# Kernel tuning notes

Hardware: AMD Instinct MI355X
Metric: run time of the kernel (lower is better)

Reference implementation:

```python
import jax, jax.numpy as jnp
import numpy as np
from jax import lax

EPS = 1e-5


def fps(xyz, npoint):
    # Farthest point sampling; xyz [B, N, 3] -> idx [B, npoint] (starts at point 0)
    B, N, _ = xyz.shape

    def body(carry, _):
        dist, far = carry
        c = jnp.take_along_axis(xyz, far[:, None, None], axis=1)  # [B,1,3]
        d = jnp.sum((xyz - c) ** 2, -1)                            # [B,N]
        dist = jnp.minimum(dist, d)
        nxt = jnp.argmax(dist, -1).astype(jnp.int32)
        return (dist, nxt), far

    init = (jnp.full((B, N), 1e10, xyz.dtype), jnp.zeros((B,), jnp.int32))
    _, idx = lax.scan(body, init, None, length=npoint)
    return idx.T  # [B, npoint]


def query_ball(radius, nsample, xyz, new_xyz):
    # xyz [B,N,3], new_xyz [B,S,3] -> idx [B,S,nsample]
    N = xyz.shape[1]
    sqr = jnp.sum((new_xyz[:, :, None, :] - xyz[:, None, :, :]) ** 2, -1)  # [B,S,N]
    idx = jnp.where(sqr > radius * radius, N, jnp.arange(N)[None, None, :])
    idx = jnp.sort(idx, axis=-1)[:, :, :nsample]
    # out-of-ball slots get replaced by the first in-ball index (torch repo behavior)
    return jnp.where(idx == N, idx[:, :, :1], idx)


def gather_pts(x, idx):
    # x [B,N,C], idx [B,...] -> [B,...,C]
    B = x.shape[0]
    b = jnp.arange(B).reshape((B,) + (1,) * (idx.ndim - 1))
    return x[b, idx]


def mlp_bn(x, layers):
    # x [B,S,K,C]; shared 1x1-conv MLP + training-mode BatchNorm + ReLU
    for w, g, b in layers:
        x = jnp.einsum('bskc,oc->bsko', x, w)
        mean = x.mean((0, 1, 2))
        var = x.var((0, 1, 2))  # biased, as torch BN uses for normalization
        x = jax.nn.relu((x - mean) * lax.rsqrt(var + EPS) * g + b)
    return x


def set_abstraction(xyz, points, npoint, radius, nsample, layers, group_all):
    B = xyz.shape[0]
    if group_all:
        new_xyz = jnp.zeros((B, 1, 3), xyz.dtype)
        new_points = xyz[:, None]  # [B,1,N,3] (raw xyz, no centering)
        if points is not None:
            new_points = jnp.concatenate([new_points, points[:, None]], -1)
    else:
        fidx = fps(xyz, npoint)
        new_xyz = gather_pts(xyz, fidx)                     # [B,S,3]
        idx = query_ball(radius, nsample, xyz, new_xyz)     # [B,S,K]
        grouped = gather_pts(xyz, idx) - new_xyz[:, :, None, :]
        if points is not None:
            new_points = jnp.concatenate([grouped, gather_pts(points, idx)], -1)
        else:
            new_points = grouped
    feat = mlp_bn(new_points, layers).max(2)  # max-pool over neighbors -> [B,S,C]
    return new_xyz, feat


def _forward(xyz_time, l1, l2, l3):
    B, T, N, _ = xyz_time.shape
    x = xyz_time.reshape(B * T, N, 4)
    xyz, t = x[..., :3], x[..., 3:]
    x1_xyz, x1 = set_abstraction(xyz, t, 512, 0.2, 32, l1, False)
    x2_xyz, x2 = set_abstraction(x1_xyz, x1, 128, 0.4, 64, l2, False)
    _, x3 = set_abstraction(x2_xyz, x2, None, None, None, l3, True)
    return x3.reshape(B, T, -1)


def setup_inputs() -> dict:
    key = jax.random.key(0)
    ks = jax.random.split(key, 16)
    inp = {"xyz_time": jax.random.uniform(ks[0], (2, 4, 4096, 4), jnp.float32)}
    specs = {1: [(64, 4), (64, 64), (128, 64)],
             2: [(128, 131), (128, 128), (256, 128)],
             3: [(256, 259), (512, 256), (1024, 512)]}
    i = 1
    for s, layers in specs.items():
        for j, (o, c) in enumerate(layers):
            inp[f"w{s}_{j}"] = jax.random.normal(jax.random.fold_in(ks[i], j), (o, c), jnp.float32) * 0.1
            inp[f"g{s}_{j}"] = jnp.ones((o,), jnp.float32)
            inp[f"b{s}_{j}"] = jnp.zeros((o,), jnp.float32)
        i += 1
    return inp


def reference(xyz_time, w1_0, g1_0, b1_0, w1_1, g1_1, b1_1, w1_2, g1_2, b1_2,
              w2_0, g2_0, b2_0, w2_1, g2_1, b2_1, w2_2, g2_2, b2_2,
              w3_0, g3_0, b3_0, w3_1, g3_1, b3_1, w3_2, g3_2, b3_2):
    l1 = [(w1_0, g1_0, b1_0), (w1_1, g1_1, b1_1), (w1_2, g1_2, b1_2)]
    l2 = [(w2_0, g2_0, b2_0), (w2_1, g2_1, b2_1), (w2_2, g2_2, b2_2)]
    l3 = [(w3_0, g3_0, b3_0), (w3_1, g3_1, b3_1), (w3_2, g3_2, b3_2)]
    return _forward(xyz_time, l1, l2, l3)
```

## Files before the change

kernel.cpp:

```cpp
#include <hip/hip_runtime.h>


typedef short s16x8 __attribute__((ext_vector_type(8)));
typedef float f32x4 __attribute__((ext_vector_type(4)));

__device__ __forceinline__ unsigned short f2bf_rne(float f) {
    unsigned u = __float_as_uint(f);
    u += 0x7FFFu + ((u >> 16) & 1u);
    return (unsigned short)(u >> 16);
}
__device__ __forceinline__ void f2bf_split(float v, unsigned short& hi,
                                           unsigned short& lo) {
    unsigned u = __float_as_uint(v);
    unsigned r = u + 0x7FFFu + ((u >> 16) & 1u);
    hi = (unsigned short)(r >> 16);
    float vh = __uint_as_float(r & 0xFFFF0000u);
    lo = f2bf_rne(v - vh);
}

__device__ __forceinline__ unsigned long long umax64(unsigned long long a,
                                                     unsigned long long b) {
    return a > b ? a : b;
}

__device__ __forceinline__ unsigned wred_umax63(unsigned v) {
    unsigned t;
    t = (unsigned)__builtin_amdgcn_update_dpp(0, (int)v, 0x111, 0xf, 0xf, true); if (t > v) v = t;
    t = (unsigned)__builtin_amdgcn_update_dpp(0, (int)v, 0x112, 0xf, 0xf, true); if (t > v) v = t;
    t = (unsigned)__builtin_amdgcn_update_dpp(0, (int)v, 0x114, 0xf, 0xf, true); if (t > v) v = t;
    t = (unsigned)__builtin_amdgcn_update_dpp(0, (int)v, 0x118, 0xf, 0xf, true); if (t > v) v = t;
    t = (unsigned)__builtin_amdgcn_update_dpp(0, (int)v, 0x142, 0xa, 0xf, true); if (t > v) v = t;
    t = (unsigned)__builtin_amdgcn_update_dpp(0, (int)v, 0x143, 0xc, 0xf, true); if (t > v) v = t;
    return v;
}

__device__ __forceinline__ void wave_argmax(unsigned dbits, unsigned nInv,
                                            unsigned& vmax, unsigned& iInv) {
    unsigned m = wred_umax63(dbits);
    vmax = (unsigned)__builtin_amdgcn_readlane((int)m, 63);
    unsigned cand = (dbits == vmax) ? nInv : 0u;
    unsigned im = wred_umax63(cand);
    iInv = (unsigned)__builtin_amdgcn_readlane((int)im, 63);
}

struct PWArgs {
    const float* w[9];
    unsigned off[9];
    int O[9], C[9], CP[9];
};
__device__ __forceinline__ void prep_w_dev(const PWArgs& a,
                                           unsigned short* __restrict__ wh,
                                           unsigned short* __restrict__ wl,
                                           int i) {
    int l = 0;
#pragma unroll
    for (int k = 1; k < 9; ++k) if (i >= (int)a.off[k]) l = k;
    int li = i - (int)a.off[l];
    int CP = a.CP[l];
    int o = li / CP;
    int c = li - o * CP;
    float v = (c < a.C[l]) ? a.w[l][(size_t)o * a.C[l] + c] : 0.f;
    unsigned short h, lo;
    f2bf_split(v, h, lo);
    wh[i] = h; wl[i] = lo;
}

template<int NT, int ITEMS, int STRIDE>
__global__ __launch_bounds__(NT) void fps_block(
    const float* __restrict__ pts, int npoint,
    int* __restrict__ outIdx, float* __restrict__ outXyz,
    int nFps, PWArgs pw, unsigned short* __restrict__ wh,
    unsigned short* __restrict__ wl, int wtotal)
{
    constexpr int N = NT * ITEMS;
    constexpr int NW = NT / 64;
    __shared__ float4 scoord[N];
    __shared__ unsigned long long wkey[2][NW];

    if (blockIdx.x >= nFps) {
        int i = (blockIdx.x - nFps) * NT + threadIdx.x;
        if (i < wtotal) prep_w_dev(pw, wh, wl, i);
        return;
    }

    const int b = blockIdx.x;
    const int tid = threadIdx.x;
    const int wid = tid >> 6;
    const int lane = tid & 63;
    const float* P = pts + (size_t)b * N * STRIDE;

    float px[ITEMS], py[ITEMS], pz[ITEMS], dloc[ITEMS];
#pragma unroll
    for (int w = 0; w < ITEMS; ++w) {
        int n = tid + w * NT;
        float x, y, z;
        if (STRIDE == 4) {
            float4 v = *(const float4*)(P + (size_t)n * 4);
            x = v.x; y = v.y; z = v.z;
        } else {
            x = P[(size_t)n * STRIDE + 0];
            y = P[(size_t)n * STRIDE + 1];
            z = P[(size_t)n * STRIDE + 2];
        }
        px[w] = x; py[w] = y; pz[w] = z;
        scoord[n] = make_float4(x, y, z, 0.f);
        dloc[w] = 1e10f;
    }
    __syncthreads();
    float4 c0 = scoord[0];
    float cx = c0.x, cy = c0.y, cz = c0.z;
    int far = 0;

    for (int i = 0; i < npoint; ++i) {
        if (tid == 0) {
            outIdx[(size_t)b * npoint + i] = far;
            outXyz[((size_t)b * npoint + i) * 3 + 0] = cx;
            outXyz[((size_t)b * npoint + i) * 3 + 1] = cy;
            outXyz[((size_t)b * npoint + i) * 3 + 2] = cz;
        }
        float bestV = -1.0f;
        int bestW = 0;
#pragma unroll
        for (int w = 0; w < ITEMS; ++w) {
            float dx = __fsub_rn(px[w], cx);
            float dy = __fsub_rn(py[w], cy);
            float dz = __fsub_rn(pz[w], cz);
            float d = __fadd_rn(__fadd_rn(__fmul_rn(dx, dx), __fmul_rn(dy, dy)),
                                __fmul_rn(dz, dz));
            float dd = fminf(dloc[w], d);
            dloc[w] = dd;
            if (dd > bestV) { bestV = dd; bestW = w; }
        }
        int bestN = tid + bestW * NT;
        unsigned vmax, iInv;
        wave_argmax(__float_as_uint(bestV), 0xFFFFFFFFu ^ (unsigned)bestN,
                    vmax, iInv);
        const int par = i & 1;
        if (lane == 0)
            wkey[par][wid] = ((unsigned long long)vmax << 32) | iInv;
        __syncthreads();
        unsigned long long kb = wkey[par][0];
#pragma unroll
        for (int w2 = 1; w2 < NW; ++w2) kb = umax64(kb, wkey[par][w2]);
        far = (int)(0xFFFFFFFFu ^ (unsigned)kb);
        float4 cc = scoord[far];
        cx = cc.x; cy = cc.y; cz = cc.z;
    }
}

__device__ void fps_wave_dev(const float* __restrict__ pts, int npoint,
                             int* __restrict__ outIdx, float* __restrict__ outXyz,
                             int b, float4* scoord)
{
    constexpr int ITEMS = 8;
    constexpr int STRIDE = 3;
    constexpr int N = 64 * ITEMS;
    const int tid = threadIdx.x;
    const float* P = pts + (size_t)b * N * STRIDE;

    float px[ITEMS], py[ITEMS], pz[ITEMS], dloc[ITEMS];
#pragma unroll
    for (int w = 0; w < ITEMS; ++w) {
        int n = tid + w * 64;
        float x = P[(size_t)n * STRIDE + 0];
        float y = P[(size_t)n * STRIDE + 1];
        float z = P[(size_t)n * STRIDE + 2];
        px[w] = x; py[w] = y; pz[w] = z;
        scoord[n] = make_float4(x, y, z, 0.f);
        dloc[w] = 1e10f;
    }
    __threadfence_block();
    float4 c0 = scoord[0];
    float cx = c0.x, cy = c0.y, cz = c0.z;
    int far = 0;

    for (int i = 0; i < npoint; ++i) {
        if (tid == 0) {
            outIdx[(size_t)b * npoint + i] = far;
            outXyz[((size_t)b * npoint + i) * 3 + 0] = cx;
            outXyz[((size_t)b * npoint + i) * 3 + 1] = cy;
            outXyz[((size_t)b * npoint + i) * 3 + 2] = cz;
        }
        float bestV = -1.0f;
        int bestW = 0;
#pragma unroll
        for (int w = 0; w < ITEMS; ++w) {
            float dx = __fsub_rn(px[w], cx);
            float dy = __fsub_rn(py[w], cy);
            float dz = __fsub_rn(pz[w], cz);
            float d = __fadd_rn(__fadd_rn(__fmul_rn(dx, dx), __fmul_rn(dy, dy)),
                                __fmul_rn(dz, dz));
            float dd = fminf(dloc[w], d);
            dloc[w] = dd;
            if (dd > bestV) { bestV = dd; bestW = w; }
        }
        int bestN = tid + bestW * 64;
        unsigned vmax, iInv;
        wave_argmax(__float_as_uint(bestV), 0xFFFFFFFFu ^ (unsigned)bestN,
                    vmax, iInv);
        far = (int)(0xFFFFFFFFu ^ iInv);
        float4 cc = scoord[far];
        cx = cc.x; cy = cc.y; cz = cc.z;
    }
}

__global__ __launch_bounds__(256) void qb_group1(
    const float* __restrict__ xyz ,
    const float* __restrict__ ctr ,
    float* __restrict__ out ,
    int nQb, const float* __restrict__ fpsPts,
    int* __restrict__ fpsIdx, float* __restrict__ fpsXyz)
{
    __shared__ float4 scoord[512];
    if ((int)blockIdx.x >= nQb) {
        if (threadIdx.x < 64)
            fps_wave_dev(fpsPts, 128, fpsIdx, fpsXyz,
                         (int)blockIdx.x - nQb, scoord);
        return;
    }
    int gw = (blockIdx.x * 256 + threadIdx.x) >> 6;
    int lane = threadIdx.x & 63;
    if (gw >= 4096) return;
    int b = gw >> 9;
    const float* P = xyz + (size_t)b * 4096 * 4;
    float cx = ctr[(size_t)gw * 3 + 0];
    float cy = ctr[(size_t)gw * 3 + 1];
    float cz = ctr[(size_t)gw * 3 + 2];
    float* out0 = out + (size_t)gw * 32 * 8;
    int cnt = 0;
    float f0x = 0.f, f0y = 0.f, f0z = 0.f, f0t = 0.f;
    bool haveFirst = false;
    for (int base = 0; base < 4096 && cnt < 32; base += 64) {
        int n = base + lane;
        float4 p = *(const float4*)(P + (size_t)n * 4);
        float ex = __fsub_rn(p.x, cx);
        float ey = __fsub_rn(p.y, cy);
        float ez = __fsub_rn(p.z, cz);
        float d = __fadd_rn(__fadd_rn(__fmul_rn(ex, ex), __fmul_rn(ey, ey)),
                            __fmul_rn(ez, ez));
        bool inb = !(d > 0.04f);
        unsigned long long mask = __ballot(inb);
        if (mask) {
            if (!haveFirst) {
                int fl = (int)__builtin_ctzll(mask);
                f0x = __shfl(ex, fl); f0y = __shfl(ey, fl);
                f0z = __shfl(ez, fl); f0t = __shfl(p.w, fl);
                haveFirst = true;
            }
            if (inb) {
                int pos = cnt + __builtin_popcountll(mask & ((1ull << lane) - 1ull));
                if (pos < 32) {
                    float* o = out0 + (size_t)pos * 8;
                    *(float4*)o = make_float4(ex, ey, ez, p.w);
                    *(float4*)(o + 4) = make_float4(0.f, 0.f, 0.f, 0.f);
                }
            }
            cnt += (int)__builtin_popcountll(mask);
        }
    }
    if (cnt > 32) cnt = 32;
    for (int p2 = cnt + lane; p2 < 32; p2 += 64) {
        float* o = out0 + (size_t)p2 * 8;
        *(float4*)o = make_float4(f0x, f0y, f0z, f0t);
        *(float4*)(o + 4) = make_float4(0.f, 0.f, 0.f, 0.f);
    }
}

__device__ __forceinline__ void qb2_dev(
    const float* __restrict__ xyz, const float* __restrict__ centers,
    int* __restrict__ outIdx, int gw, int lane)
{
    const int N = 512, stride = 3, S = 128, nsample = 64;
    const float r2 = 0.16f;
    int b = gw / S;
    const float* P = xyz + (size_t)b * N * stride;
    float cx = centers[(size_t)gw * 3 + 0];
    float cy = centers[(size_t)gw * 3 + 1];
    float cz = centers[(size_t)gw * 3 + 2];
    int* out = outIdx + (size_t)gw * nsample;
    int cnt = 0;
    int firstIdx = 0;
    bool haveFirst = false;
    for (int base = 0; base < N && cnt < nsample; base += 64) {
        int n = base + lane;
        bool inb = false;
        if (n < N) {
            float dx = __fsub_rn(cx, P[(size_t)n * stride + 0]);
            float dy = __fsub_rn(cy, P[(size_t)n * stride + 1]);
            float dz = __fsub_rn(cz, P[(size_t)n * stride + 2]);
            float d = __fadd_rn(__fadd_rn(__fmul_rn(dx, dx), __fmul_rn(dy, dy)),
                                __fmul_rn(dz, dz));
            inb = !(d > r2);
        }
        unsigned long long mask = __ballot(inb);
        if (mask) {
            if (!haveFirst) { firstIdx = base + __builtin_ctzll(mask); haveFirst = true; }
            if (inb) {
                int pos = cnt + __builtin_popcountll(mask & ((1ull << lane) - 1ull));
                if (pos < nsample) out[pos] = n;
            }
            cnt += (int)__builtin_popcountll(mask);
        }
    }
    if (cnt > nsample) cnt = nsample;
    for (int p = cnt + lane; p < nsample; p += 64) out[p] = firstIdx;
}

__global__ __launch_bounds__(256) void gemm_fused(
    const float* __restrict__ X,
    const double* __restrict__ pSin, const double* __restrict__ pQin,
    const float* __restrict__ gIn, const float* __restrict__ bIn,
    double invMin, int applyAct,
    const unsigned short* __restrict__ Bh, const unsigned short* __restrict__ Bl,
    float* __restrict__ Y,
    double* __restrict__ pSout, double* __restrict__ pQout,
    int AC, int CPW, int O, int gmode,
    const int* __restrict__ gqb, const float* __restrict__ gxyz,
    const float* __restrict__ gctr, const float* __restrict__ gfeat)
{
    constexpr int PITCH = 40;
    __shared__ __align__(16) unsigned short sAh[128 * PITCH];
    __shared__ __align__(16) unsigned short sAl[128 * PITCH];
    __shared__ __align__(16) unsigned short sBh[128 * PITCH];
    __shared__ __align__(16) unsigned short sBl[128 * PITCH];
    __shared__ float sred[2048];
    __shared__ float sScale[512];
    __shared__ float sShift[512];

    const int tid = threadIdx.x;
    const int lane = tid & 63;
    const int wid = tid >> 6;
    const int col15 = lane & 15;
    const int quad = lane >> 4;
    const int wm = (wid >> 1) * 64;
    const int wo = (wid & 1) * 64;
    const int m0 = blockIdx.x * 128;
    const int o0 = blockIdx.y * 128;
    const int lr = tid >> 2;
    const int lc = (tid & 3) * 8;

    if (applyAct) {
        for (int c = tid; c < AC; c += 256) {
            double S = pSin[c], Q = pQin[c];
            double mean = S * invMin;
            double var = Q * invMin - mean * mean;
            float varf = (float)var;
            if (varf < 0.f) varf = 0.f;
            float sc = gIn[c] * rsqrtf(varf + 1e-5f);
            sScale[c] = sc;
            sShift[c] = bIn[c] - (float)mean * sc;
        }
    }
    __syncthreads();

    f32x4 acc[4][4];
#pragma unroll
    for (int mt = 0; mt < 4; ++mt)
#pragma unroll
        for (int ot = 0; ot < 4; ++ot)
            acc[mt][ot] = {0.f, 0.f, 0.f, 0.f};

    for (int k0 = 0; k0 < CPW; k0 += 32) {
#pragma unroll
        for (int it = 0; it < 2; ++it) {
            int r = lr + it * 64;
            int c = k0 + lc;
            unsigned short h[8], l[8];
            float vv[8];
            bool have = true;
            if (gmode == 0) {
                if (c + 8 <= AC) {
                    const float* xr = X + (size_t)(m0 + r) * AC + c;
                    float4 v0 = *(const float4*)xr;
                    float4 v1 = *(const float4*)(xr + 4);
                    vv[0] = v0.x; vv[1] = v0.y; vv[2] = v0.z; vv[3] = v0.w;
                    vv[4] = v1.x; vv[5] = v1.y; vv[6] = v1.z; vv[7] = v1.w;
                    if (applyAct) {
#pragma unroll
                        for (int j = 0; j < 8; ++j)
                            vv[j] = fmaxf(vv[j] * sScale[c + j] + sShift[c + j], 0.f);
                    }
                } else {
                    have = false;
                }
            } else if (gmode == 2) {
                int m = m0 + r;
                int idx = gqb[m];
                idx = (idx < 0) ? 0 : (idx > 511 ? 511 : idx);
                int bb2 = m >> 13;
                int bs = m >> 6;
                const float* frow = gfeat + ((size_t)bb2 * 512 + idx) * 128;
                const float* xrow = gxyz + ((size_t)bb2 * 512 + idx) * 3;
                const float* crow = gctr + (size_t)bs * 3;
#pragma unroll
                for (int j = 0; j < 8; ++j) {
                    int cc = c + j;
                    float v = 0.f;
                    if (cc < 3)        v = __fsub_rn(xrow[cc], crow[cc]);
                    else if (cc < 131) v = frow[cc - 3];
                    vv[j] = v;
                }
            } else {
                int m = m0 + r;
                const float* frow = gfeat + (size_t)m * 256;
                const float* crow = gctr + (size_t)m * 3;
#pragma unroll
                for (int j = 0; j < 8; ++j) {
                    int cc = c + j;
                    float v = 0.f;
                    if (cc < 3)        v = crow[cc];
                    else if (cc < 259) v = frow[cc - 3];
                    vv[j] = v;
                }
            }
            if (have) {
#pragma unroll
                for (int j = 0; j < 8; ++j) f2bf_split(vv[j], h[j], l[j]);
            } else {
#pragma unroll
                for (int j = 0; j < 8; ++j) { h[j] = 0; l[j] = 0; }
            }
            *(ushort4*)&sAh[r * PITCH + lc] = make_ushort4(h[0], h[1], h[2], h[3]);
            *(ushort4*)&sAh[r * PITCH + lc + 4] = make_ushort4(h[4], h[5], h[6], h[7]);
            *(ushort4*)&sAl[r * PITCH + lc] = make_ushort4(l[0], l[1], l[2], l[3]);
            *(ushort4*)&sAl[r * PITCH + lc + 4] = make_ushort4(l[4], l[5], l[6], l[7]);
        }
#pragma unroll
        for (int it = 0; it < 2; ++it) {
            int r = lr + it * 64;
            int c = k0 + lc;
            int o = o0 + r;
            uint4 vh = {0, 0, 0, 0}, vl = {0, 0, 0, 0};
            if (o < O && c < CPW) {
                size_t goff = (size_t)o * CPW + c;
                vh = *(const uint4*)(Bh + goff);
                vl = *(const uint4*)(Bl + goff);
            }
            *(uint4*)&sBh[r * PITCH + lc] = vh;
            *(uint4*)&sBl[r * PITCH + lc] = vl;
        }
        __syncthreads();
        s16x8 ah[4], al[4], bh[4], bl[4];
#pragma unroll
        for (int mt = 0; mt < 4; ++mt) {
            int rowoff = (wm + mt * 16 + col15) * PITCH + quad * 8;
            ah[mt] = *(const s16x8*)&sAh[rowoff];
            al[mt] = *(const s16x8*)&sAl[rowoff];
        }
#pragma unroll
        for (int ot = 0; ot < 4; ++ot) {
            int rowoff = (wo + ot * 16 + col15) * PITCH + quad * 8;
            bh[ot] = *(const s16x8*)&sBh[rowoff];
            bl[ot] = *(const s16x8*)&sBl[rowoff];
        }
#pragma unroll
        for (int mt = 0; mt < 4; ++mt)
#pragma unroll
            for (int ot = 0; ot < 4; ++ot) {
                acc[mt][ot] = __builtin_amdgcn_mfma_f32_16x16x32_bf16(
                    ah[mt], bl[ot], acc[mt][ot], 0, 0, 0);
                acc[mt][ot] = __builtin_amdgcn_mfma_f32_16x16x32_bf16(
                    al[mt], bh[ot], acc[mt][ot], 0, 0, 0);
                acc[mt][ot] = __builtin_amdgcn_mfma_f32_16x16x32_bf16(
                    ah[mt], bh[ot], acc[mt][ot], 0, 0, 0);
            }
        __syncthreads();
    }
#pragma unroll
    for (int mt = 0; mt < 4; ++mt)
#pragma unroll
        for (int ot = 0; ot < 4; ++ot) {
            int og = o0 + wo + ot * 16 + col15;
            if (og < O) {
#pragma unroll
                for (int r = 0; r < 4; ++r) {
                    int mg = m0 + wm + mt * 16 + quad * 4 + r;
                    Y[(size_t)mg * O + og] = acc[mt][ot][r];
                }
            }
        }
#pragma unroll
    for (int ot = 0; ot < 4; ++ot) {
        float s = 0.f, s2 = 0.f;
#pragma unroll
        for (int mt = 0; mt < 4; ++mt)
#pragma unroll
            for (int r = 0; r < 4; ++r) {
                float v = acc[mt][ot][r];
                s += v;
                s2 += v * v;
            }
        int slot = ((wid * 4 + quad) * 16 + col15) * 4 + ot;
        sred[slot * 2] = s;
        sred[slot * 2 + 1] = s2;
    }
    __syncthreads();
    if (tid < 128) {
        int col = tid;
        int o = o0 + col;
        if (o < O) {
            int cb = col >> 6;
            int ot = (col & 63) >> 4;
            int c15 = col & 15;
            double S = 0.0, S2 = 0.0;
#pragma unroll
            for (int wp = 0; wp < 2; ++wp) {
                int wd = cb + wp * 2;
#pragma unroll
                for (int q = 0; q < 4; ++q) {
                    int slot = ((wd * 4 + q) * 16 + c15) * 4 + ot;
                    S += (double)sred[slot * 2];
                    S2 += (double)sred[slot * 2 + 1];
                }
            }
            atomicAdd(&pSout[o], S);
            atomicAdd(&pQout[o], S2);
        }
    }
}

__global__ __launch_bounds__(256) void bn_relu_max(
    const float* __restrict__ Y,
    const double* __restrict__ pS, const double* __restrict__ pQ,
    const float* __restrict__ gv, const float* __restrict__ bv, double invM,
    float* __restrict__ out, int Stot, int K, int O, int nMain,
    const float* __restrict__ qbXyz, const float* __restrict__ qbCtr,
    int* __restrict__ qbOut)
{
    if ((int)blockIdx.x >= nMain) {
        int wid = threadIdx.x >> 6, lane = threadIdx.x & 63;
        int gw = ((int)blockIdx.x - nMain) * 4 + wid;
        if (gw < 1024) qb2_dev(qbXyz, qbCtr, qbOut, gw, lane);
        return;
    }
    int idx = blockIdx.x * 256 + threadIdx.x;
    if (idx >= Stot * O) return;
    int s = idx / O;
    int o = idx - s * O;
    double S = pS[o], Q = pQ[o];
    double mean = S * invM;
    double var = Q * invM - mean * mean;
    float varf = (float)var;
    if (varf < 0.f) varf = 0.f;
    float sc = gv[o] * rsqrtf(varf + 1e-5f);
    float sh = bv[o] - (float)mean * sc;
    const float* basep = Y + (size_t)s * K * O + o;
    float mx = 0.f;
    for (int k = 0; k < K; ++k) {
        float v = basep[(size_t)k * O] * sc + sh;
        v = fmaxf(v, 0.f);
        mx = fmaxf(mx, v);
    }
    out[idx] = mx;
}

extern "C" void kernel_launch(void* const* d_in, const int* in_sizes, int n_in,
                              void* d_out, int out_size, void* d_ws, size_t ws_size,
                              hipStream_t stream)
{
    const float* xin = (const float*)d_in[0];
    const float* w[9]; const float* g[9]; const float* bb[9];
    for (int i = 0; i < 9; ++i) {
        w[i]  = (const float*)d_in[1 + 3 * i];
        g[i]  = (const float*)d_in[2 + 3 * i];
        bb[i] = (const float*)d_in[3 + 3 * i];
    }

    char* base = (char*)d_ws;
    size_t off = 0;
    auto alloc = [&](size_t bytes) -> void* {
        void* p = base + off;
        off = (off + bytes + 255) & ~(size_t)255;
        return p;
    };
    const int OC[9][3] = {{64,4,8},{64,64,64},{128,64,64},
                          {128,131,136},{128,128,128},{256,128,128},
                          {256,259,264},{512,256,256},{1024,512,512}};
    size_t woff[10]; woff[0] = 0;
    for (int i = 0; i < 9; ++i) woff[i + 1] = woff[i] + (size_t)OC[i][0] * OC[i][2];

    int*    fps1   = (int*)alloc((size_t)4096 * 4);
    int*    fps2   = (int*)alloc((size_t)1024 * 4);
    int*    qb2    = (int*)alloc((size_t)65536 * 4);
    float*  nx1    = (float*)alloc((size_t)12288 * 4);
    float*  nx2    = (float*)alloc((size_t)3072 * 4);
    float*  feat1  = (float*)alloc((size_t)524288 * 4);
    float*  feat2  = (float*)alloc((size_t)262144 * 4);
    double* partS  = (double*)alloc((size_t)9 * 1024 * 8);
    double* partQ  = (double*)alloc((size_t)9 * 1024 * 8);
    unsigned short* WH = (unsigned short*)alloc(woff[9] * 2);
    unsigned short* WL = (unsigned short*)alloc(woff[9] * 2);
    const size_t zeroBytes = off;
    float*  XG = (float*)alloc((size_t)65536 * 136 * 4);
    float*  A  = (float*)alloc((size_t)16777216 * 4);
    if (off > ws_size) return;

    hipMemsetAsync(d_ws, 0, zeroBytes, stream);

    PWArgs pwa;
    for (int i = 0; i < 9; ++i) {
        pwa.w[i] = w[i]; pwa.off[i] = (unsigned)woff[i];
        pwa.O[i] = OC[i][0]; pwa.C[i] = OC[i][1]; pwa.CP[i] = OC[i][2];
    }
    const int nPrep = (int)((woff[9] + 255) / 256);

    auto gemm = [&](const float* X, int prevLi, double invMprev, int li,
                    float* Y, int YB, int OB, int AC, int CPW, int O,
                    int gmode, const int* gqb, const float* gxyz,
                    const float* gctr, const float* gfeat) {
        gemm_fused<<<dim3(YB, OB), 256, 0, stream>>>(
            X,
            prevLi >= 0 ? partS + (size_t)prevLi * 1024 : nullptr,
            prevLi >= 0 ? partQ + (size_t)prevLi * 1024 : nullptr,
            prevLi >= 0 ? g[prevLi] : nullptr,
            prevLi >= 0 ? bb[prevLi] : nullptr,
            invMprev, prevLi >= 0 ? 1 : 0,
            WH + woff[li], WL + woff[li], Y,
            partS + (size_t)li * 1024, partQ + (size_t)li * 1024,
            AC, CPW, O, gmode, gqb, gxyz, gctr, gfeat);
    };

    const double inv1 = 1.0 / 131072.0;
    const double inv2 = 1.0 / 65536.0;
    const double inv3 = 1.0 / 1024.0;

    fps_block<256, 16, 4><<<8 + nPrep, 256, 0, stream>>>(
        xin, 512, fps1, nx1, 8, pwa, WH, WL, (int)woff[9]);
    qb_group1<<<1024 + 8, 256, 0, stream>>>(xin, nx1, XG, 1024, nx1, fps2, nx2);

    gemm(XG, -1, 0.0, 0, A, 1024, 1, 8, 8, 64, 0, nullptr, nullptr, nullptr, nullptr);
    gemm(A, 0, inv1, 1, XG, 1024, 1, 64, 64, 64, 0, nullptr, nullptr, nullptr, nullptr);
    gemm(XG, 1, inv1, 2, A, 1024, 1, 64, 64, 128, 0, nullptr, nullptr, nullptr, nullptr);
    bn_relu_max<<<2048 + 256, 256, 0, stream>>>(
        A, partS + 2 * 1024, partQ + 2 * 1024, g[2], bb[2], inv1,
        feat1, 4096, 32, 128, 2048, nx1, nx2, qb2);

    gemm(nullptr, -1, 0.0, 3, A, 512, 1, 136, 136, 128, 2, qb2, nx1, nx2, feat1);
    gemm(A, 3, inv2, 4, XG, 512, 1, 128, 128, 128, 0, nullptr, nullptr, nullptr, nullptr);
    gemm(XG, 4, inv2, 5, A, 512, 2, 128, 128, 256, 0, nullptr, nullptr, nullptr, nullptr);
    bn_relu_max<<<(1024 * 256) / 256, 256, 0, stream>>>(
        A, partS + 5 * 1024, partQ + 5 * 1024, g[5], bb[5], inv2,
        feat2, 1024, 64, 256, 1024 * 256 / 256, nullptr, nullptr, nullptr);

    gemm(nullptr, -1, 0.0, 6, A, 8, 2, 264, 264, 256, 3, nullptr, nullptr, nx2, feat2);
    gemm(A, 6, inv3, 7, XG, 8, 4, 256, 256, 512, 0, nullptr, nullptr, nullptr, nullptr);
    gemm(XG, 7, inv3, 8, A, 8, 8, 512, 512, 1024, 0, nullptr, nullptr, nullptr, nullptr);
    bn_relu_max<<<(8 * 1024) / 256, 256, 0, stream>>>(
        A, partS + 8 * 1024, partQ + 8 * 1024, g[8], bb[8], inv3,
        (float*)d_out, 8, 128, 1024, (8 * 1024) / 256,
        nullptr, nullptr, nullptr);
}
```

Before: 826.9 us.

## Fuse per-group max/min pooling into final GEMM epilogue of SA1 and SA2

The last GEMM of set-abstraction levels 1 and 2 no longer writes the full pre-activation tensor. It reduces each group of K samples to a per-channel max and min in registers, using cross-lane shuffles, and stores only those. bn_relu_max then picks max or min depending on the sign of the BN scale and applies the affine transform and ReLU, which avoids the large write and reread of the [S*K, O] intermediate. This relies on the affine-then-ReLU being monotonic per channel, and on each 64-row warp tile lining up with group boundaries.

```diff
diff --git a/kernel.cpp b/kernel.cpp
--- a/kernel.cpp
+++ b/kernel.cpp
@@ -316,7 +316,8 @@
     double* __restrict__ pSout, double* __restrict__ pQout,
     int AC, int CPW, int O, int gmode,
     const int* __restrict__ gqb, const float* __restrict__ gxyz,
-    const float* __restrict__ gctr, const float* __restrict__ gfeat)
+    const float* __restrict__ gctr, const float* __restrict__ gfeat,
+    int redK, float* __restrict__ Vmax, float* __restrict__ Vmin)
 {
     constexpr int PITCH = 40;
     __shared__ __align__(16) unsigned short sAh[128 * PITCH];
@@ -466,19 +467,72 @@
             }
         __syncthreads();
     }
-#pragma unroll
-    for (int mt = 0; mt < 4; ++mt)
+    if (redK == 0) {
+#pragma unroll
+        for (int mt = 0; mt < 4; ++mt)
+#pragma unroll
+            for (int ot = 0; ot < 4; ++ot) {
+                int og = o0 + wo + ot * 16 + col15;
+                if (og < O) {
+#pragma unroll
+                    for (int r = 0; r < 4; ++r) {
+                        int mg = m0 + wm + mt * 16 + quad * 4 + r;
+                        Y[(size_t)mg * O + og] = acc[mt][ot][r];
+                    }
+                }
+            }
+    } else if (redK == 32) {
 #pragma unroll
         for (int ot = 0; ot < 4; ++ot) {
             int og = o0 + wo + ot * 16 + col15;
-            if (og < O) {
+#pragma unroll
+            for (int cp = 0; cp < 2; ++cp) {
+                float mx = acc[2 * cp][ot][0];
+                float mn = mx;
+#pragma unroll
+                for (int mi = 0; mi < 2; ++mi)
+#pragma unroll
+                    for (int r = 0; r < 4; ++r) {
+                        float v = acc[2 * cp + mi][ot][r];
+                        mx = fmaxf(mx, v);
+                        mn = fminf(mn, v);
+                    }
+                mx = fmaxf(mx, __shfl_xor(mx, 16));
+                mx = fmaxf(mx, __shfl_xor(mx, 32));
+                mn = fminf(mn, __shfl_xor(mn, 16));
+                mn = fminf(mn, __shfl_xor(mn, 32));
+                if (quad == 0) {
+                    int ctr = (m0 >> 5) + (wm >> 5) + cp;
+                    Vmax[(size_t)ctr * O + og] = mx;
+                    Vmin[(size_t)ctr * O + og] = mn;
+                }
+            }
+        }
+    } else {
+#pragma unroll
+        for (int ot = 0; ot < 4; ++ot) {
+            int og = o0 + wo + ot * 16 + col15;
+            float mx = acc[0][ot][0];
+            float mn = mx;
+#pragma unroll
+            for (int mt = 0; mt < 4; ++mt)
 #pragma unroll
                 for (int r = 0; r < 4; ++r) {
-                    int mg = m0 + wm + mt * 16 + quad * 4 + r;
-                    Y[(size_t)mg * O + og] = acc[mt][ot][r];
+                    float v = acc[mt][ot][r];
+                    mx = fmaxf(mx, v);
+                    mn = fminf(mn, v);
                 }
-            }
-        }
+            mx = fmaxf(mx, __shfl_xor(mx, 16));
+            mx = fmaxf(mx, __shfl_xor(mx, 32));
+            mn = fminf(mn, __shfl_xor(mn, 16));
+            mn = fminf(mn, __shfl_xor(mn, 32));
+            if (quad == 0) {
+                int ctr = (m0 >> 6) + (wm >> 6);
+                Vmax[(size_t)ctr * O + og] = mx;
+                Vmin[(size_t)ctr * O + og] = mn;
+            }
+        }
+    }
 #pragma unroll
     for (int ot = 0; ot < 4; ++ot) {
         float s = 0.f, s2 = 0.f;
@@ -520,10 +574,10 @@
 }
 
 __global__ __launch_bounds__(256) void bn_relu_max(
-    const float* __restrict__ Y,
+    const float* __restrict__ Y, const float* __restrict__ Vmin,
     const double* __restrict__ pS, const double* __restrict__ pQ,
     const float* __restrict__ gv, const float* __restrict__ bv, double invM,
-    float* __restrict__ out, int Stot, int K, int O, int nMain,
+    float* __restrict__ out, int Stot, int K, int O, int vmode, int nMain,
     const float* __restrict__ qbXyz, const float* __restrict__ qbCtr,
     int* __restrict__ qbOut)
 {
@@ -544,6 +598,13 @@
     if (varf < 0.f) varf = 0.f;
     float sc = gv[o] * rsqrtf(varf + 1e-5f);
     float sh = bv[o] - (float)mean * sc;
+    if (vmode) {
+        float vmax = Y[(size_t)s * O + o];
+        float vmin = Vmin[(size_t)s * O + o];
+        float v = (sc >= 0.f) ? vmax : vmin;
+        out[idx] = fmaxf(v * sc + sh, 0.f);
+        return;
+    }
     const float* basep = Y + (size_t)s * K * O + o;
     float mx = 0.f;
     for (int k = 0; k < K; ++k) {
@@ -607,7 +668,8 @@
     auto gemm = [&](const float* X, int prevLi, double invMprev, int li,
                     float* Y, int YB, int OB, int AC, int CPW, int O,
                     int gmode, const int* gqb, const float* gxyz,
-                    const float* gctr, const float* gfeat) {
+                    const float* gctr, const float* gfeat,
+                    int redK, float* Vmax, float* Vmin) {
         gemm_fused<<<dim3(YB, OB), 256, 0, stream>>>(
             X,
             prevLi >= 0 ? partS + (size_t)prevLi * 1024 : nullptr,
@@ -617,7 +679,7 @@
             invMprev, prevLi >= 0 ? 1 : 0,
             WH + woff[li], WL + woff[li], Y,
             partS + (size_t)li * 1024, partQ + (size_t)li * 1024,
-            AC, CPW, O, gmode, gqb, gxyz, gctr, gfeat);
+            AC, CPW, O, gmode, gqb, gxyz, gctr, gfeat, redK, Vmax, Vmin);
     };
 
     const double inv1 = 1.0 / 131072.0;
@@ -628,25 +690,25 @@
         xin, 512, fps1, nx1, 8, pwa, WH, WL, (int)woff[9]);
     qb_group1<<<1024 + 8, 256, 0, stream>>>(xin, nx1, XG, 1024, nx1, fps2, nx2);
 
-    gemm(XG, -1, 0.0, 0, A, 1024, 1, 8, 8, 64, 0, nullptr, nullptr, nullptr, nullptr);
-    gemm(A, 0, inv1, 1, XG, 1024, 1, 64, 64, 64, 0, nullptr, nullptr, nullptr, nullptr);
-    gemm(XG, 1, inv1, 2, A, 1024, 1, 64, 64, 128, 0, nullptr, nullptr, nullptr, nullptr);
+    gemm(XG, -1, 0.0, 0, A, 1024, 1, 8, 8, 64, 0, nullptr, nullptr, nullptr, nullptr, 0, nullptr, nullptr);
+    gemm(A, 0, inv1, 1, XG, 1024, 1, 64, 64, 64, 0, nullptr, nullptr, nullptr, nullptr, 0, nullptr, nullptr);
+    gemm(XG, 1, inv1, 2, A, 1024, 1, 64, 64, 128, 0, nullptr, nullptr, nullptr, nullptr, 32, A, A + 524288);
     bn_relu_max<<<2048 + 256, 256, 0, stream>>>(
-        A, partS + 2 * 1024, partQ + 2 * 1024, g[2], bb[2], inv1,
-        feat1, 4096, 32, 128, 2048, nx1, nx2, qb2);
-
-    gemm(nullptr, -1, 0.0, 3, A, 512, 1, 136, 136, 128, 2, qb2, nx1, nx2, feat1);
-    gemm(A, 3, inv2, 4, XG, 512, 1, 128, 128, 128, 0, nullptr, nullptr, nullptr, nullptr);
-    gemm(XG, 4, inv2, 5, A, 512, 2, 128, 128, 256, 0, nullptr, nullptr, nullptr, nullptr);
+        A, A + 524288, partS + 2 * 1024, partQ + 2 * 1024, g[2], bb[2], inv1,
+        feat1, 4096, 32, 128, 1, 2048, nx1, nx2, qb2);
+
+    gemm(nullptr, -1, 0.0, 3, A, 512, 1, 136, 136, 128, 2, qb2, nx1, nx2, feat1, 0, nullptr, nullptr);
+    gemm(A, 3, inv2, 4, XG, 512, 1, 128, 128, 128, 0, nullptr, nullptr, nullptr, nullptr, 0, nullptr, nullptr);
+    gemm(XG, 4, inv2, 5, A, 512, 2, 128, 128, 256, 0, nullptr, nullptr, nullptr, nullptr, 64, A, A + 262144);
     bn_relu_max<<<(1024 * 256) / 256, 256, 0, stream>>>(
-        A, partS + 5 * 1024, partQ + 5 * 1024, g[5], bb[5], inv2,
-        feat2, 1024, 64, 256, 1024 * 256 / 256, nullptr, nullptr, nullptr);
-
-    gemm(nullptr, -1, 0.0, 6, A, 8, 2, 264, 264, 256, 3, nullptr, nullptr, nx2, feat2);
-    gemm(A, 6, inv3, 7, XG, 8, 4, 256, 256, 512, 0, nullptr, nullptr, nullptr, nullptr);
-    gemm(XG, 7, inv3, 8, A, 8, 8, 512, 512, 1024, 0, nullptr, nullptr, nullptr, nullptr);
+        A, A + 262144, partS + 5 * 1024, partQ + 5 * 1024, g[5], bb[5], inv2,
+        feat2, 1024, 64, 256, 1, 1024 * 256 / 256, nullptr, nullptr, nullptr);
+
+    gemm(nullptr, -1, 0.0, 6, A, 8, 2, 264, 264, 256, 3, nullptr, nullptr, nx2, feat2, 0, nullptr, nullptr);
+    gemm(A, 6, inv3, 7, XG, 8, 4, 256, 256, 512, 0, nullptr, nullptr, nullptr, nullptr, 0, nullptr, nullptr);
+    gemm(XG, 7, inv3, 8, A, 8, 8, 512, 512, 1024, 0, nullptr, nullptr, nullptr, nullptr, 0, nullptr, nullptr);
     bn_relu_max<<<(8 * 1024) / 256, 256, 0, stream>>>(
-        A, partS + 8 * 1024, partQ + 8 * 1024, g[8], bb[8], inv3,
-        (float*)d_out, 8, 128, 1024, (8 * 1024) / 256,
+        A, nullptr, partS + 8 * 1024, partQ + 8 * 1024, g[8], bb[8], inv3,
+        (float*)d_out, 8, 128, 1024, 0, (8 * 1024) / 256,
         nullptr, nullptr, nullptr);
 }
```

Result: faster. 794.8 us (-3.9%).
